# Kernel tuning notes

Hardware: AMD Instinct MI355X
Metric: run time of the kernel (lower is better)

The kernel has to match this reference:

```python
import jax, jax.numpy as jnp
import numpy as np

NUM_STEPS = 50   # global num_steps in source
SCALE = 1000     # global scale in source (fc1 out / fc2 in)
SUBTHRESH = 0.5  # HeavisideBoxcar surrogate half-width
THRESH = 1.0     # firing threshold

@jax.custom_vjp
def heaviside_boxcar(x):
    # spike = H(x); surrogate grad = boxcar of half-width SUBTHRESH
    return (x >= 0.0).astype(x.dtype)

def _hb_fwd(x):
    return heaviside_boxcar(x), x

def _hb_bwd(x, g):
    return (g * (jnp.abs(x) < SUBTHRESH).astype(g.dtype),)

heaviside_boxcar.defvjp(_hb_fwd, _hb_bwd)


def setup_inputs() -> dict:
    key = jax.random.key(0)
    k1, k2, k3 = jax.random.split(key, 3)
    B = 1024
    x = jax.random.uniform(k1, (B, 784), dtype=jnp.float32)  # pixel intensities in [0,1]
    W1 = jax.random.normal(k2, (SCALE, 784), jnp.float32) / np.sqrt(784).astype(np.float32)
    W2 = jax.random.normal(k3, (100, SCALE), jnp.float32) / np.sqrt(SCALE).astype(np.float32)
    tau_0 = jnp.array([2.0], jnp.float32)       # sigmoid(2) ~ 0.88 decay
    tau_vector = jnp.array([2.0], jnp.float32)
    acc_tau = jnp.array([2.0], jnp.float32)
    return {"x": x, "W1": W1, "W2": W2, "tau_0": tau_0,
            "tau_vector": tau_vector, "acc_tau": acc_tau}


def reference(x, W1, W2, tau_0, tau_vector, acc_tau):
    B = x.shape[0]
    # snn.spikegen.rate: per-step Bernoulli(p=x) spikes, shape [T, B, 784]
    u = jax.random.uniform(jax.random.key(42), (NUM_STEPS, B, 784), dtype=x.dtype)
    x_spk = (u < x[None]).astype(x.dtype)

    decay_0 = jax.nn.sigmoid(tau_0[0])
    decay_v = jax.nn.sigmoid(tau_vector[0])
    acc_decay = jax.nn.sigmoid(acc_tau[0])

    h1_mem = jnp.full((B, SCALE), 0.5, x.dtype)
    h1_spk = jnp.zeros((B, SCALE), x.dtype)
    h2_mem = jnp.full((B, 100), 0.5, x.dtype)
    h2_spk = jnp.zeros((B, 100), x.dtype)
    acc = jnp.zeros((B, 10), x.dtype)

    def step(carry, xt):
        h1m, h1s, h2m, h2s, acc = carry
        # pPLIF: mem = mem*decay*(1-spk) + I ; spike = H(mem - thresh)
        h1m = h1m * decay_0 * (1.0 - h1s) + xt @ W1.T
        h1s = heaviside_boxcar(h1m - THRESH)
        h2m = h2m * decay_v * (1.0 - h2s) + h1s @ W2.T
        h2s = heaviside_boxcar(h2m - THRESH)
        boost = jnp.mean(h2s.reshape(B, 10, 10), axis=2)  # AvgPool1d(10,10)
        acc = acc * acc_decay + boost                      # pPLI accumulator
        return (h1m, h1s, h2m, h2s, acc), None

    carry, _ = jax.lax.scan(step, (h1_mem, h1_spk, h2_mem, h2_spk, acc),
                            x_spk[:NUM_STEPS - 1])
    # torch loop runs under no_grad with detach(): block grads through it
    h1m, h1s, h2m, h2s, acc = jax.tree_util.tree_map(jax.lax.stop_gradient, carry)

    # final, differentiable step
    h1m = h1m * decay_0 * (1.0 - h1s) + x_spk[NUM_STEPS - 1] @ W1.T
    h1s = heaviside_boxcar(h1m - THRESH)
    h2m = h2m * decay_v * (1.0 - h2s) + h1s @ W2.T
    h2s = heaviside_boxcar(h2m - THRESH)
    boost = jnp.mean(h2s.reshape(B, 10, 10), axis=2)
    acc = acc * acc_decay + boost
    return acc
```

## Files before the change

### kernel.cpp

```cpp
#include <hip/hip_runtime.h>
#include <hip/hip_bf16.h>
#include <math.h>


#define NSTEPS 50
#define KC1 25
#define NSL 5

typedef __attribute__((ext_vector_type(4)))  int i32x4;
typedef __attribute__((ext_vector_type(16))) int i32x16;

#define OFF_B1     0ull
#define OFF_B2     5111808ull
#define OFF_H1MST  5898240ull
#define OFF_H1SST  14286848ull
#define OFF_H2MST  15335424ull
#define OFF_H2SST  16384000ull
#define OFF_ACCST  16515072ull
#define OFF_AF     16596992ull
#define FIXED_END  59195392ull
#define PERSTEP    8388608ull

#define PREP_BLOCKS 19200

__device__ __forceinline__ unsigned int rotl32(unsigned int v, int d) {
#if __has_builtin(__builtin_amdgcn_alignbit)
  return __builtin_amdgcn_alignbit(v, v, (unsigned int)(32 - d));
#else
  return (v << d) | (v >> (32 - d));
#endif
}

__device__ __forceinline__ unsigned int tf_bits(unsigned int i) {
  const unsigned int ks0 = 0u;
  const unsigned int ks1 = 42u;
  const unsigned int ks2 = 0x1BD11BDAu ^ 0u ^ 42u;
  unsigned int x0 = 0u + ks0;
  unsigned int x1 = i + ks1;
#define TF_RND(r) { x0 += x1; x1 = rotl32(x1, r); x1 ^= x0; }
  TF_RND(13) TF_RND(15) TF_RND(26) TF_RND(6)
  x0 += ks1; x1 += ks2 + 1u;
  TF_RND(17) TF_RND(29) TF_RND(16) TF_RND(24)
  x0 += ks2; x1 += ks0 + 2u;
  TF_RND(13) TF_RND(15) TF_RND(26) TF_RND(6)
  x0 += ks0; x1 += ks1 + 3u;
  TF_RND(17) TF_RND(29) TF_RND(16) TF_RND(24)
  x0 += ks1; x1 += ks2 + 4u;
  TF_RND(13) TF_RND(15) TF_RND(26) TF_RND(6)
  x0 += ks2; x1 += ks0 + 5u;
#undef TF_RND
  return x0 ^ x1;
}

__device__ __forceinline__ void spike_block(
    const float* __restrict__ x, i32x4* __restrict__ A, int t0, int gblk,
    int tid) {
  int g = gblk * 4 + (tid >> 6);
  int lane = tid & 63;
  int kc = g % 25;
  int r = g / 25;
  int mt = r & 31;
  int t = t0 + (r >> 5);
  int b = mt * 32 + (lane & 31);
  int j0 = kc * 32 + ((lane >> 5) << 4);
  unsigned int wds[4] = {0u, 0u, 0u, 0u};
  if (j0 < 784) {
    unsigned int base = (unsigned int)(t * 1024 + b) * 784u + (unsigned int)j0;
    const float* xp = x + b * 784 + j0;
#pragma unroll
    for (int q = 0; q < 4; ++q) {
      float4 xv = *(const float4*)(xp + 4 * q);
      unsigned int K0 = (unsigned int)(int)ceilf(xv.x * 8388608.0f);
      unsigned int K1 = (unsigned int)(int)ceilf(xv.y * 8388608.0f);
      unsigned int K2 = (unsigned int)(int)ceilf(xv.z * 8388608.0f);
      unsigned int K3 = (unsigned int)(int)ceilf(xv.w * 8388608.0f);
      unsigned int w4 = 0u;
      if ((tf_bits(base + 4 * q + 0) >> 9) < K0) w4 |= 1u;
      if ((tf_bits(base + 4 * q + 1) >> 9) < K1) w4 |= 1u << 8;
      if ((tf_bits(base + 4 * q + 2) >> 9) < K2) w4 |= 1u << 16;
      if ((tf_bits(base + 4 * q + 3) >> 9) < K3) w4 |= 1u << 24;
      wds[q] = w4;
    }
  }
  i32x4 v;
  v.x = (int)wds[0]; v.y = (int)wds[1]; v.z = (int)wds[2]; v.w = (int)wds[3];
  A[(size_t)(((t * 32 + mt) * 26) + kc) * 64 + lane] = v;
}

__global__ __launch_bounds__(256) void setup_kernel(
    const float* __restrict__ W1, const float* __restrict__ W2,
    signed char* __restrict__ B1, signed char* __restrict__ B2,
    const float* __restrict__ x, i32x4* __restrict__ A) {
  if (blockIdx.x >= PREP_BLOCKS) {
    spike_block(x, A, 0, blockIdx.x - PREP_BLOCKS, threadIdx.x);
    return;
  }
  int idx = blockIdx.x * 256 + threadIdx.x;
  const int NB1 = NSL * 32 * 26 * 1024;
  const int NB2 = NSL * 4 * 32 * 1024;
  float w;
  int s;
  signed char* dst;
  if (idx < NB1) {
    int jj = idx & 15;
    int lane = (idx >> 4) & 63;
    int kc = (idx >> 10) % 26;
    int rest = (idx >> 10) / 26;
    int nt = rest & 31;
    s = rest >> 5;
    int k = kc * 32 + ((lane >> 5) << 4) + jj;
    int o = nt * 32 + (lane & 31);
    w = (o < 1000 && k < 784) ? W1[o * 784 + k] : 0.0f;
    dst = B1 + idx;
  } else {
    int m = idx - NB1;
    if (m >= NB2) return;
    int jj = m & 15;
    int lane = (m >> 4) & 63;
    int kc = (m >> 10) & 31;
    int rest = (m >> 10) >> 5;
    int nt = rest & 3;
    s = rest >> 2;
    int k = kc * 32 + ((lane >> 5) << 4) + jj;
    int o = nt * 32 + (lane & 31);
    w = (o < 100 && k < 1000) ? W2[o * 1000 + k] : 0.0f;
    dst = B2 + m;
  }
  long long V = llrint((double)w * 281474976710656.0);
  signed char d = 0;
  for (int q = 0; q <= s + 1; ++q) {
    d = (signed char)(V & 0xFF);
    V = (V - (long long)d) >> 8;
  }
  *dst = d;
}

__global__ __launch_bounds__(256, 2) void gemm1_kernel(
    const signed char* __restrict__ Bf, const signed char* __restrict__ Afc,
    int* __restrict__ T1L, short* __restrict__ T1H) {
  __shared__ i32x4 bls[2][NSL][64];
  int tid = threadIdx.x, lane = tid & 63, wv = tid >> 6;
  int id = blockIdx.x;
  int low5 = id & 31;
  int nt = ((low5 & 7) << 2) | ((low5 >> 3) & 3);
  int mg = id >> 5;
  int tl = mg >> 2;
  int q  = mg & 3;
  int mtA = q * 8 + wv * 2;
  const i32x4* ApA = (const i32x4*)Afc + (size_t)((tl * 32 + mtA) * 26) * 64 + lane;
  const i32x4* ApB = ApA + 26 * 64;
  const i32x4* Bp = (const i32x4*)Bf + lane;
#define B1_IDX(s, kc) ((size_t)(((s) * 32 + nt) * 26 + (kc)) * 64)
  const bool st4 = (wv == 0);

  i32x16 CA[NSL], CB[NSL];
#pragma unroll
  for (int s = 0; s < NSL; ++s)
#pragma unroll
    for (int i = 0; i < 16; ++i) { CA[s][i] = 0; CB[s][i] = 0; }

  i32x4 sa = Bp[B1_IDX(wv, 0)];
  i32x4 sb; if (st4) sb = Bp[B1_IDX(4, 0)];
  i32x4 aA0 = ApA[0], aB0 = ApB[0];
  i32x4 aA1 = ApA[64], aB1 = ApB[64];
  i32x4 aA2, aB2;
  bls[0][wv][lane] = sa;
  if (st4) bls[0][4][lane] = sb;
  sa = Bp[B1_IDX(wv, 1)];
  if (st4) sb = Bp[B1_IDX(4, 1)];
  __syncthreads();

  for (int kc = 0; kc < KC1; ++kc) {
    const int cur = kc & 1, nxt = cur ^ 1;
    if (kc + 1 < KC1) {
      bls[nxt][wv][lane] = sa;
      if (st4) bls[nxt][4][lane] = sb;
    }
    if (kc + 2 < KC1) {
      sa = Bp[B1_IDX(wv, kc + 2)];
      if (st4) sb = Bp[B1_IDX(4, kc + 2)];
      aA2 = ApA[(size_t)(kc + 2) * 64];
      aB2 = ApB[(size_t)(kc + 2) * 64];
    }
#pragma unroll
    for (int s = 0; s < NSL; ++s) {
      i32x4 b = bls[cur][s][lane];
      CA[s] = __builtin_amdgcn_mfma_i32_32x32x32_i8(aA0, b, CA[s], 0, 0, 0);
      CB[s] = __builtin_amdgcn_mfma_i32_32x32x32_i8(aB0, b, CB[s], 0, 0, 0);
    }
    __syncthreads();
    aA0 = aA1; aA1 = aA2;
    aB0 = aB1; aB1 = aB2;
  }

  int o = nt * 32 + (lane & 31);
  int rb = 4 * (lane >> 5);
#pragma unroll
  for (int r = 0; r < 16; ++r) {
    int row = (r & 3) + 8 * (r >> 2) + rb;
    long long TA = (long long)CA[4][r];
    TA = (TA << 8) + (long long)CA[3][r];
    TA = (TA << 8) + (long long)CA[2][r];
    TA = (TA << 8) + (long long)CA[1][r];
    TA = (TA << 8) + (long long)CA[0][r];
    long long TB = (long long)CB[4][r];
    TB = (TB << 8) + (long long)CB[3][r];
    TB = (TB << 8) + (long long)CB[2][r];
    TB = (TB << 8) + (long long)CB[1][r];
    TB = (TB << 8) + (long long)CB[0][r];
    int bA = mtA * 32 + row;
    size_t i0 = ((size_t)tl * 1024 + bA) * 1024 + o;
    size_t i1 = ((size_t)tl * 1024 + bA + 32) * 1024 + o;
    T1L[i0] = (int)TA;
    T1H[i0] = (short)(TA >> 32);
    T1L[i1] = (int)TB;
    T1H[i1] = (short)(TB >> 32);
  }
}

__global__ __launch_bounds__(256) void rec1_kernel(
    const int* __restrict__ T1L, const short* __restrict__ T1H,
    signed char* __restrict__ h1sc,
    double* __restrict__ h1m_st, signed char* __restrict__ h1s_st,
    const float* __restrict__ tau0, int t0, int C,
    const float* __restrict__ x, i32x4* __restrict__ A, int t1) {
  if (blockIdx.x >= 512) {
    spike_block(x, A, t1, blockIdx.x - 512, threadIdx.x);
    return;
  }
  int tid = threadIdx.x;
  int lane = tid & 63, sub = tid >> 6;
  int b = blockIdx.x * 2 + (sub >> 1);
  int obase = (sub & 1) * 512 + lane;
  double alpha = 1.0 / (1.0 + exp(-(double)tau0[0]));
  double m[8], s[8];
  if (t0 == 0) {
#pragma unroll
    for (int j = 0; j < 8; ++j) { m[j] = 0.5; s[j] = 0.0; }
  } else {
#pragma unroll
    for (int j = 0; j < 8; ++j) {
      m[j] = h1m_st[(size_t)b * 1024 + obase + 64 * j];
      s[j] = (double)h1s_st[(size_t)b * 1024 + obase + 64 * j];
    }
  }
  for (int tl = 0; tl < C; ++tl) {
    const int*   Lp = T1L + ((size_t)tl * 1024 + b) * 1024 + obase;
    const short* Hp = T1H + ((size_t)tl * 1024 + b) * 1024 + obase;
    signed char* Sp = h1sc + ((size_t)tl * 1024 + b) * 1024 + obase;
#pragma unroll
    for (int j = 0; j < 8; ++j) {
      long long T = ((long long)Hp[64 * j] << 32) +
                    (long long)(unsigned int)Lp[64 * j];
      double I = (double)T * 0x1p-40;
      m[j] = (s[j] != 0.0 ? 0.0 : m[j] * alpha) + I;
      bool sp = (m[j] - 1.0) >= 0.0;
      s[j] = sp ? 1.0 : 0.0;
      Sp[64 * j] = sp ? 1 : 0;
    }
  }
#pragma unroll
  for (int j = 0; j < 8; ++j) {
    h1m_st[(size_t)b * 1024 + obase + 64 * j] = m[j];
    h1s_st[(size_t)b * 1024 + obase + 64 * j] = (signed char)(s[j] != 0.0 ? 1 : 0);
  }
}

__global__ __launch_bounds__(256, 3) void gemm2_kernel(
    const signed char* __restrict__ Bf, const signed char* __restrict__ h1sc,
    double* __restrict__ T2, int ngemm,
    const float* __restrict__ x, i32x4* __restrict__ A, int t1, int gofs) {
  if ((int)blockIdx.x >= ngemm) {
    spike_block(x, A, t1, gofs + (int)blockIdx.x - ngemm, threadIdx.x);
    return;
  }
  __shared__ i32x4 bls[2][NSL][64];
  int tid = threadIdx.x, lane = tid & 63, wv = tid >> 6;
  int nt = blockIdx.x & 3;
  int mg = blockIdx.x >> 2;
  int tl = mg >> 3;
  int mt = ((mg & 7) << 2) + wv;
  const signed char* Arow =
      h1sc + ((size_t)tl * 1024 + mt * 32 + (lane & 31)) * 1024 + ((lane >> 5) << 4);
  const i32x4* Bp = (const i32x4*)Bf + lane;
  const bool st4 = (wv == 0);
#define B2_IDX(s, kc) ((size_t)(((s) * 4 + nt) * 32 + (kc)) * 64)

  i32x16 C[NSL];
#pragma unroll
  for (int s = 0; s < NSL; ++s)
#pragma unroll
    for (int i = 0; i < 16; ++i) C[s][i] = 0;

  i32x4 sa = Bp[B2_IDX(wv, 0)];
  i32x4 sb; if (st4) sb = Bp[B2_IDX(4, 0)];
  i32x4 a0 = *(const i32x4*)(Arow);
  i32x4 a1 = *(const i32x4*)(Arow + 32);
  i32x4 a2;
  bls[0][wv][lane] = sa;
  if (st4) bls[0][4][lane] = sb;
  sa = Bp[B2_IDX(wv, 1)];
  if (st4) sb = Bp[B2_IDX(4, 1)];
  __syncthreads();

  for (int kc = 0; kc < 32; ++kc) {
    const int cur = kc & 1, nxt = cur ^ 1;
    if (kc + 1 < 32) {
      bls[nxt][wv][lane] = sa;
      if (st4) bls[nxt][4][lane] = sb;
    }
    if (kc + 2 < 32) {
      sa = Bp[B2_IDX(wv, kc + 2)];
      if (st4) sb = Bp[B2_IDX(4, kc + 2)];
      a2 = *(const i32x4*)(Arow + (size_t)(kc + 2) * 32);
    }
    i32x4 b0 = bls[cur][0][lane], b1 = bls[cur][1][lane], b2 = bls[cur][2][lane];
    i32x4 b3 = bls[cur][3][lane], b4 = bls[cur][4][lane];
    C[0] = __builtin_amdgcn_mfma_i32_32x32x32_i8(a0, b0, C[0], 0, 0, 0);
    C[1] = __builtin_amdgcn_mfma_i32_32x32x32_i8(a0, b1, C[1], 0, 0, 0);
    C[2] = __builtin_amdgcn_mfma_i32_32x32x32_i8(a0, b2, C[2], 0, 0, 0);
    C[3] = __builtin_amdgcn_mfma_i32_32x32x32_i8(a0, b3, C[3], 0, 0, 0);
    C[4] = __builtin_amdgcn_mfma_i32_32x32x32_i8(a0, b4, C[4], 0, 0, 0);
    a0 = a1; a1 = a2;
    __syncthreads();
  }

  int o = nt * 32 + (lane & 31);
  int rb = 4 * (lane >> 5);
#pragma unroll
  for (int r = 0; r < 16; ++r) {
    int row = (r & 3) + 8 * (r >> 2) + rb;
    int b = mt * 32 + row;
    long long T = (long long)C[4][r];
    T = (T << 8) + (long long)C[3][r];
    T = (T << 8) + (long long)C[2][r];
    T = (T << 8) + (long long)C[1][r];
    T = (T << 8) + (long long)C[0][r];
    T2[((size_t)tl * 1024 + b) * 128 + o] = (double)T * 0x1p-40;
  }
}

__global__ __launch_bounds__(256) void rec2_kernel(
    const double* __restrict__ T2, double* __restrict__ h2m_st,
    signed char* __restrict__ h2s_st, double* __restrict__ acc_st,
    const float* __restrict__ tauv, const float* __restrict__ acct,
    int t0, int C, float* __restrict__ out) {
  __shared__ signed char sp[256];
  int tid = threadIdx.x;
  int b = blockIdx.x * 2 + (tid >> 7);
  int o = tid & 127;
  double alpha = 1.0 / (1.0 + exp(-(double)tauv[0]));
  double adec  = 1.0 / (1.0 + exp(-(double)acct[0]));
  double m, s, accv = 0.0;
  bool isPool = (o < 10);
  if (t0 == 0) {
    m = 0.5; s = 0.0;
  } else {
    m = h2m_st[(size_t)b * 128 + o];
    s = (double)h2s_st[(size_t)b * 128 + o];
    if (isPool) accv = acc_st[b * 10 + o];
  }
  for (int tl = 0; tl < C; ++tl) {
    double I = T2[((size_t)tl * 1024 + b) * 128 + o];
    m = (s != 0.0 ? 0.0 : m * alpha) + I;
    bool spk = (m - 1.0) >= 0.0;
    s = spk ? 1.0 : 0.0;
    sp[tid] = spk ? 1 : 0;
    __syncthreads();
    if (isPool) {
      int base = tid & 128;
      int isum = 0;
#pragma unroll
      for (int k = 0; k < 10; ++k) isum += sp[base + o * 10 + k];
      accv = accv * adec + (double)isum / 10.0;
      if (t0 + tl == NSTEPS - 1) out[b * 10 + o] = (float)accv;
    }
    __syncthreads();
  }
  h2m_st[(size_t)b * 128 + o] = m;
  h2s_st[(size_t)b * 128 + o] = (signed char)(s != 0.0 ? 1 : 0);
  if (isPool) acc_st[b * 10 + o] = accv;
}

extern "C" void kernel_launch(void* const* d_in, const int* in_sizes, int n_in,
                              void* d_out, int out_size, void* d_ws, size_t ws_size,
                              hipStream_t stream) {
  const float* x    = (const float*)d_in[0];
  const float* W1   = (const float*)d_in[1];
  const float* W2   = (const float*)d_in[2];
  const float* tau0 = (const float*)d_in[3];
  const float* tauv = (const float*)d_in[4];
  const float* acct = (const float*)d_in[5];
  float* out = (float*)d_out;
  char*  ws  = (char*)d_ws;

  signed char* B1     = (signed char*)(ws + OFF_B1);
  signed char* B2     = (signed char*)(ws + OFF_B2);
  double*      h1m_st = (double*)(ws + OFF_H1MST);
  signed char* h1s_st = (signed char*)(ws + OFF_H1SST);
  double*      h2m_st = (double*)(ws + OFF_H2MST);
  signed char* h2s_st = (signed char*)(ws + OFF_H2SST);
  double*      acc_st = (double*)(ws + OFF_ACCST);
  signed char* Af     = (signed char*)(ws + OFF_AF);
  i32x4*       Afv    = (i32x4*)Af;

  long long avail = (long long)ws_size - (long long)FIXED_END;
  int C = (int)(avail / (long long)PERSTEP);
  if (C < 1) C = 1;
  if (C > 13) C = 13;
  size_t off_t1l  = FIXED_END;
  size_t off_t1h  = off_t1l + (size_t)C * 4194304ull;
  size_t off_h1sc = off_t1h + (size_t)C * 2097152ull;
  size_t off_t2   = off_h1sc + (size_t)C * 1048576ull;
  int*         T1L  = (int*)(ws + off_t1l);
  short*       T1H  = (short*)(ws + off_t1h);
  signed char* h1sc = (signed char*)(ws + off_h1sc);
  double*      T2   = (double*)(ws + off_t2);

  int C0 = (C < NSTEPS) ? C : NSTEPS;
  setup_kernel<<<PREP_BLOCKS + C0 * 200, 256, 0, stream>>>(
      W1, W2, B1, B2, x, Afv);

  for (int t0 = 0; t0 < NSTEPS; t0 += C) {
    int Cc = (NSTEPS - t0 < C) ? (NSTEPS - t0) : C;
    int t1 = t0 + Cc;
    int Cn = (t1 < NSTEPS) ? ((NSTEPS - t1 < C) ? (NSTEPS - t1) : C) : 0;
    int spkTot = Cn * 200;
    int spkA = spkTot / 2;
    int spkB = spkTot - spkA;
    int ngemm2 = 4 * Cc * 8;

    gemm1_kernel<<<32 * Cc * 4, 256, 0, stream>>>(
        B1, Af + (size_t)t0 * 851968ull, T1L, T1H);
    rec1_kernel<<<512 + spkA, 256, 0, stream>>>(
        T1L, T1H, h1sc, h1m_st, h1s_st, tau0, t0, Cc, x, Afv, t1);
    gemm2_kernel<<<ngemm2 + spkB, 256, 0, stream>>>(
        B2, h1sc, T2, ngemm2, x, Afv, t1, spkA);
    rec2_kernel<<<512, 256, 0, stream>>>(
        T2, h2m_st, h2s_st, acc_st, tauv, acct, t0, Cc, out);
  }
}
```

Baseline: 486.4 us.

## Fuse layer-1 GEMM with recurrence in persistent LDS-resident weight kernel

Replaces the chunked gemm1/rec1 kernel pair with one persistent kernel. Each block keeps its W1 column-tile slices in dynamic shared memory, loops over all 50 timesteps, and applies the membrane/spike recurrence in registers, overlapped with the next step's MFMAs through double-buffered accumulators. This removes the 48-bit T1L/T1H intermediate round-trip to global memory and most kernel launches, and gemm2/rec2 now run once over all steps. In exchange only 256 blocks run the layer-1 chain serially per step. The workspace grows to a fixed large size, and all spike inputs are generated up front in setup.

Measured after the change: 1.298 ms. 2.67x slower.

```diff
diff --git a/kernel.cpp b/kernel.cpp
--- a/kernel.cpp
+++ b/kernel.cpp
@@ -11,17 +11,16 @@
 typedef __attribute__((ext_vector_type(16))) int i32x16;
 
 #define OFF_B1     0ull
-#define OFF_B2     5111808ull
-#define OFF_H1MST  5898240ull
-#define OFF_H1SST  14286848ull
-#define OFF_H2MST  15335424ull
-#define OFF_H2SST  16384000ull
-#define OFF_ACCST  16515072ull
-#define OFF_AF     16596992ull
-#define FIXED_END  59195392ull
-#define PERSTEP    8388608ull
-
-#define PREP_BLOCKS 19200
+#define OFF_B2     4259840ull
+#define OFF_AF     4915200ull
+#define OFF_H1SC   47513600ull
+#define OFF_T2     99942400ull
+#define OFF_H2M    152371200ull
+#define OFF_H2S    153419776ull
+#define OFF_ACC    153550848ull
+#define WS_END     153632768ull
+
+#define PREP_BLOCKS 3840
 
 __device__ __forceinline__ unsigned int rotl32(unsigned int v, int d) {
 #if __has_builtin(__builtin_amdgcn_alignbit)
@@ -96,184 +95,133 @@
     return;
   }
   int idx = blockIdx.x * 256 + threadIdx.x;
-  const int NB1 = NSL * 32 * 26 * 1024;
-  const int NB2 = NSL * 4 * 32 * 1024;
+  const int NB1 = 32 * 26 * 64 * 16;
   float w;
-  int s;
   signed char* dst;
+  size_t stride;
   if (idx < NB1) {
     int jj = idx & 15;
     int lane = (idx >> 4) & 63;
     int kc = (idx >> 10) % 26;
-    int rest = (idx >> 10) / 26;
-    int nt = rest & 31;
-    s = rest >> 5;
+    int nt = (idx >> 10) / 26;
     int k = kc * 32 + ((lane >> 5) << 4) + jj;
     int o = nt * 32 + (lane & 31);
     w = (o < 1000 && k < 784) ? W1[o * 784 + k] : 0.0f;
-    dst = B1 + idx;
+    dst = B1 + (size_t)(nt * 26 + kc) * 5120 + (lane << 4) + jj;
+    stride = 1024;
   } else {
-    int m = idx - NB1;
-    if (m >= NB2) return;
-    int jj = m & 15;
-    int lane = (m >> 4) & 63;
-    int kc = (m >> 10) & 31;
-    int rest = (m >> 10) >> 5;
-    int nt = rest & 3;
-    s = rest >> 2;
+    int m2 = idx - NB1;
+    int jj = m2 & 15;
+    int lane = (m2 >> 4) & 63;
+    int kc = (m2 >> 10) & 31;
+    int nt = (m2 >> 10) >> 5;
     int k = kc * 32 + ((lane >> 5) << 4) + jj;
     int o = nt * 32 + (lane & 31);
     w = (o < 100 && k < 1000) ? W2[o * 1000 + k] : 0.0f;
-    dst = B2 + m;
+    dst = B2 + (size_t)(nt * 32 + kc) * 1024 + (lane << 4) + jj;
+    stride = 4 * 32 * 1024;
   }
   long long V = llrint((double)w * 281474976710656.0);
-  signed char d = 0;
-  for (int q = 0; q <= s + 1; ++q) {
+  signed char d = (signed char)(V & 0xFF);
+  V = (V - (long long)d) >> 8;
+#pragma unroll
+  for (int s = 0; s < 5; ++s) {
     d = (signed char)(V & 0xFF);
     V = (V - (long long)d) >> 8;
-  }
-  *dst = d;
-}
-
-__global__ __launch_bounds__(256, 2) void gemm1_kernel(
-    const signed char* __restrict__ Bf, const signed char* __restrict__ Afc,
-    int* __restrict__ T1L, short* __restrict__ T1H) {
-  __shared__ i32x4 bls[2][NSL][64];
-  int tid = threadIdx.x, lane = tid & 63, wv = tid >> 6;
-  int id = blockIdx.x;
-  int low5 = id & 31;
-  int nt = ((low5 & 7) << 2) | ((low5 >> 3) & 3);
-  int mg = id >> 5;
-  int tl = mg >> 2;
-  int q  = mg & 3;
-  int mtA = q * 8 + wv * 2;
-  const i32x4* ApA = (const i32x4*)Afc + (size_t)((tl * 32 + mtA) * 26) * 64 + lane;
-  const i32x4* ApB = ApA + 26 * 64;
-  const i32x4* Bp = (const i32x4*)Bf + lane;
-#define B1_IDX(s, kc) ((size_t)(((s) * 32 + nt) * 26 + (kc)) * 64)
-  const bool st4 = (wv == 0);
-
-  i32x16 CA[NSL], CB[NSL];
-#pragma unroll
-  for (int s = 0; s < NSL; ++s)
+    dst[(size_t)s * stride] = d;
+  }
+}
+
+#define F1_EPI(CP, r) do {                                                    \
+    long long T = (long long)CP[4][r];                                        \
+    T = (T << 8) + (long long)CP[3][r];                                       \
+    T = (T << 8) + (long long)CP[2][r];                                       \
+    T = (T << 8) + (long long)CP[1][r];                                       \
+    T = (T << 8) + (long long)CP[0][r];                                       \
+    double I = (double)T * 0x1p-40;                                           \
+    double mm = (((spk >> (r)) & 1u) ? 0.0 : m[r] * alpha) + I;               \
+    m[r] = mm;                                                                \
+    unsigned int sp = (mm >= 1.0) ? 1u : 0u;                                  \
+    spk = (spk & ~(1u << (r))) | (sp << (r));                                 \
+    hp[(size_t)(((r) & 3) + 8 * ((r) >> 2) + rb) * 1024] = (signed char)sp;   \
+    CP[0][r] = 0; CP[1][r] = 0; CP[2][r] = 0; CP[3][r] = 0; CP[4][r] = 0;     \
+  } while (0)
+
+#define F1_PHASE(CC, CP, DOEPI) do {                                          \
+    _Pragma("unroll")                                                         \
+    for (int kc = 0; kc < 25; ++kc) {                                         \
+      i32x4 b0 = blsv[(kc * 4 + 0) * 64 + lane];                              \
+      i32x4 b1 = blsv[(kc * 4 + 1) * 64 + lane];                              \
+      i32x4 b2 = blsv[(kc * 4 + 2) * 64 + lane];                              \
+      i32x4 b3 = blsv[(kc * 4 + 3) * 64 + lane];                              \
+      i32x4 av = a0, gv = g0;                                                 \
+      a0 = a1; g0 = g1;                                                       \
+      a1 = (kc + 2 < 25) ? Ap[(kc + 2) * 64]                                  \
+                         : Ap[53248 + (kc + 2 - 25) * 64];                    \
+      g1 = (kc + 2 < 25) ? Bg[((kc + 2) * 5 + 4) * 64]                        \
+                         : Bg[((kc + 2 - 25) * 5 + 4) * 64];                  \
+      CC[0] = __builtin_amdgcn_mfma_i32_32x32x32_i8(av, b0, CC[0], 0, 0, 0);  \
+      CC[1] = __builtin_amdgcn_mfma_i32_32x32x32_i8(av, b1, CC[1], 0, 0, 0);  \
+      CC[2] = __builtin_amdgcn_mfma_i32_32x32x32_i8(av, b2, CC[2], 0, 0, 0);  \
+      CC[3] = __builtin_amdgcn_mfma_i32_32x32x32_i8(av, b3, CC[3], 0, 0, 0);  \
+      CC[4] = __builtin_amdgcn_mfma_i32_32x32x32_i8(av, gv, CC[4], 0, 0, 0);  \
+      if ((DOEPI) && kc < 16) F1_EPI(CP, kc);                                 \
+    }                                                                         \
+    Ap += 53248;                                                              \
+    if (DOEPI) hp += 1048576;                                                 \
+  } while (0)
+
+__global__ __launch_bounds__(256, 1) void fused1_kernel(
+    const signed char* __restrict__ B1, const i32x4* __restrict__ Afc,
+    signed char* __restrict__ h1sc, const float* __restrict__ tau0) {
+  extern __shared__ i32x4 blsv[];
+  const int tid = threadIdx.x, lane = tid & 63, wv = tid >> 6;
+  const int id = (int)blockIdx.x;
+  const int mtg = id & 7, nt = id >> 3;
+  const int mt = mtg * 4 + wv;
+  const i32x4* B1v = (const i32x4*)B1;
+
+  for (int r = tid; r < 6400; r += 256) {
+    int fi = r >> 6, l = r & 63;
+    int kc = fi >> 2, s = fi & 3;
+    blsv[r] = B1v[(size_t)nt * 8320 + (kc * 5 + s) * 64 + l];
+  }
+
+  const double alpha = 1.0 / (1.0 + exp(-(double)tau0[0]));
+  double m[16];
+  unsigned int spk = 0;
+#pragma unroll
+  for (int r = 0; r < 16; ++r) m[r] = 0.5;
+  i32x16 CA[5], CB[5];
+#pragma unroll
+  for (int s = 0; s < 5; ++s)
 #pragma unroll
     for (int i = 0; i < 16; ++i) { CA[s][i] = 0; CB[s][i] = 0; }
 
-  i32x4 sa = Bp[B1_IDX(wv, 0)];
-  i32x4 sb; if (st4) sb = Bp[B1_IDX(4, 0)];
-  i32x4 aA0 = ApA[0], aB0 = ApB[0];
-  i32x4 aA1 = ApA[64], aB1 = ApB[64];
-  i32x4 aA2, aB2;
-  bls[0][wv][lane] = sa;
-  if (st4) bls[0][4][lane] = sb;
-  sa = Bp[B1_IDX(wv, 1)];
-  if (st4) sb = Bp[B1_IDX(4, 1)];
+  const i32x4* Ap = Afc + (size_t)mt * 26 * 64 + lane;
+  const i32x4* Bg = B1v + (size_t)nt * 8320 + lane;
+  const int rb = 4 * (lane >> 5);
+  signed char* hp = h1sc + (size_t)(mt * 32) * 1024 + nt * 32 + (lane & 31);
+
   __syncthreads();
 
-  for (int kc = 0; kc < KC1; ++kc) {
-    const int cur = kc & 1, nxt = cur ^ 1;
-    if (kc + 1 < KC1) {
-      bls[nxt][wv][lane] = sa;
-      if (st4) bls[nxt][4][lane] = sb;
-    }
-    if (kc + 2 < KC1) {
-      sa = Bp[B1_IDX(wv, kc + 2)];
-      if (st4) sb = Bp[B1_IDX(4, kc + 2)];
-      aA2 = ApA[(size_t)(kc + 2) * 64];
-      aB2 = ApB[(size_t)(kc + 2) * 64];
-    }
-#pragma unroll
-    for (int s = 0; s < NSL; ++s) {
-      i32x4 b = bls[cur][s][lane];
-      CA[s] = __builtin_amdgcn_mfma_i32_32x32x32_i8(aA0, b, CA[s], 0, 0, 0);
-      CB[s] = __builtin_amdgcn_mfma_i32_32x32x32_i8(aB0, b, CB[s], 0, 0, 0);
-    }
-    __syncthreads();
-    aA0 = aA1; aA1 = aA2;
-    aB0 = aB1; aB1 = aB2;
-  }
-
-  int o = nt * 32 + (lane & 31);
-  int rb = 4 * (lane >> 5);
-#pragma unroll
-  for (int r = 0; r < 16; ++r) {
-    int row = (r & 3) + 8 * (r >> 2) + rb;
-    long long TA = (long long)CA[4][r];
-    TA = (TA << 8) + (long long)CA[3][r];
-    TA = (TA << 8) + (long long)CA[2][r];
-    TA = (TA << 8) + (long long)CA[1][r];
-    TA = (TA << 8) + (long long)CA[0][r];
-    long long TB = (long long)CB[4][r];
-    TB = (TB << 8) + (long long)CB[3][r];
-    TB = (TB << 8) + (long long)CB[2][r];
-    TB = (TB << 8) + (long long)CB[1][r];
-    TB = (TB << 8) + (long long)CB[0][r];
-    int bA = mtA * 32 + row;
-    size_t i0 = ((size_t)tl * 1024 + bA) * 1024 + o;
-    size_t i1 = ((size_t)tl * 1024 + bA + 32) * 1024 + o;
-    T1L[i0] = (int)TA;
-    T1H[i0] = (short)(TA >> 32);
-    T1L[i1] = (int)TB;
-    T1H[i1] = (short)(TB >> 32);
-  }
-}
-
-__global__ __launch_bounds__(256) void rec1_kernel(
-    const int* __restrict__ T1L, const short* __restrict__ T1H,
-    signed char* __restrict__ h1sc,
-    double* __restrict__ h1m_st, signed char* __restrict__ h1s_st,
-    const float* __restrict__ tau0, int t0, int C,
-    const float* __restrict__ x, i32x4* __restrict__ A, int t1) {
-  if (blockIdx.x >= 512) {
-    spike_block(x, A, t1, blockIdx.x - 512, threadIdx.x);
-    return;
-  }
-  int tid = threadIdx.x;
-  int lane = tid & 63, sub = tid >> 6;
-  int b = blockIdx.x * 2 + (sub >> 1);
-  int obase = (sub & 1) * 512 + lane;
-  double alpha = 1.0 / (1.0 + exp(-(double)tau0[0]));
-  double m[8], s[8];
-  if (t0 == 0) {
-#pragma unroll
-    for (int j = 0; j < 8; ++j) { m[j] = 0.5; s[j] = 0.0; }
-  } else {
-#pragma unroll
-    for (int j = 0; j < 8; ++j) {
-      m[j] = h1m_st[(size_t)b * 1024 + obase + 64 * j];
-      s[j] = (double)h1s_st[(size_t)b * 1024 + obase + 64 * j];
-    }
-  }
-  for (int tl = 0; tl < C; ++tl) {
-    const int*   Lp = T1L + ((size_t)tl * 1024 + b) * 1024 + obase;
-    const short* Hp = T1H + ((size_t)tl * 1024 + b) * 1024 + obase;
-    signed char* Sp = h1sc + ((size_t)tl * 1024 + b) * 1024 + obase;
-#pragma unroll
-    for (int j = 0; j < 8; ++j) {
-      long long T = ((long long)Hp[64 * j] << 32) +
-                    (long long)(unsigned int)Lp[64 * j];
-      double I = (double)T * 0x1p-40;
-      m[j] = (s[j] != 0.0 ? 0.0 : m[j] * alpha) + I;
-      bool sp = (m[j] - 1.0) >= 0.0;
-      s[j] = sp ? 1.0 : 0.0;
-      Sp[64 * j] = sp ? 1 : 0;
-    }
-  }
-#pragma unroll
-  for (int j = 0; j < 8; ++j) {
-    h1m_st[(size_t)b * 1024 + obase + 64 * j] = m[j];
-    h1s_st[(size_t)b * 1024 + obase + 64 * j] = (signed char)(s[j] != 0.0 ? 1 : 0);
-  }
+  i32x4 a0 = Ap[0], a1 = Ap[64];
+  i32x4 g0 = Bg[4 * 64], g1 = Bg[9 * 64];
+
+  F1_PHASE(CA, CB, 0);
+#pragma unroll 1
+  for (int tp = 0; tp < 24; ++tp) {
+    F1_PHASE(CB, CA, 1);
+    F1_PHASE(CA, CB, 1);
+  }
+  F1_PHASE(CB, CA, 1);
+#pragma unroll
+  for (int r = 0; r < 16; ++r) F1_EPI(CB, r);
 }
 
 __global__ __launch_bounds__(256, 3) void gemm2_kernel(
     const signed char* __restrict__ Bf, const signed char* __restrict__ h1sc,
-    double* __restrict__ T2, int ngemm,
-    const float* __restrict__ x, i32x4* __restrict__ A, int t1, int gofs) {
-  if ((int)blockIdx.x >= ngemm) {
-    spike_block(x, A, t1, gofs + (int)blockIdx.x - ngemm, threadIdx.x);
-    return;
-  }
+    double* __restrict__ T2) {
   __shared__ i32x4 bls[2][NSL][64];
   int tid = threadIdx.x, lane = tid & 63, wv = tid >> 6;
   int nt = blockIdx.x & 3;
@@ -396,47 +344,29 @@
 
   signed char* B1     = (signed char*)(ws + OFF_B1);
   signed char* B2     = (signed char*)(ws + OFF_B2);
-  double*      h1m_st = (double*)(ws + OFF_H1MST);
-  signed char* h1s_st = (signed char*)(ws + OFF_H1SST);
-  double*      h2m_st = (double*)(ws + OFF_H2MST);
-  signed char* h2s_st = (signed char*)(ws + OFF_H2SST);
-  double*      acc_st = (double*)(ws + OFF_ACCST);
   signed char* Af     = (signed char*)(ws + OFF_AF);
+  signed char* h1sc   = (signed char*)(ws + OFF_H1SC);
+  double*      T2     = (double*)(ws + OFF_T2);
+  double*      h2m_st = (double*)(ws + OFF_H2M);
+  signed char* h2s_st = (signed char*)(ws + OFF_H2S);
+  double*      acc_st = (double*)(ws + OFF_ACC);
   i32x4*       Afv    = (i32x4*)Af;
 
-  long long avail = (long long)ws_size - (long long)FIXED_END;
-  int C = (int)(avail / (long long)PERSTEP);
-  if (C < 1) C = 1;
-  if (C > 13) C = 13;
-  size_t off_t1l  = FIXED_END;
-  size_t off_t1h  = off_t1l + (size_t)C * 4194304ull;
-  size_t off_h1sc = off_t1h + (size_t)C * 2097152ull;
-  size_t off_t2   = off_h1sc + (size_t)C * 1048576ull;
-  int*         T1L  = (int*)(ws + off_t1l);
-  short*       T1H  = (short*)(ws + off_t1h);
-  signed char* h1sc = (signed char*)(ws + off_h1sc);
-  double*      T2   = (double*)(ws + off_t2);
-
-  int C0 = (C < NSTEPS) ? C : NSTEPS;
-  setup_kernel<<<PREP_BLOCKS + C0 * 200, 256, 0, stream>>>(
+  static bool attr_done = false;
+  if (!attr_done) {
+    (void)hipFuncSetAttribute((const void*)fused1_kernel,
+                              hipFuncAttributeMaxDynamicSharedMemorySize,
+                              102400);
+    attr_done = true;
+  }
+
+  setup_kernel<<<PREP_BLOCKS + NSTEPS * 200, 256, 0, stream>>>(
       W1, W2, B1, B2, x, Afv);
 
-  for (int t0 = 0; t0 < NSTEPS; t0 += C) {
-    int Cc = (NSTEPS - t0 < C) ? (NSTEPS - t0) : C;
-    int t1 = t0 + Cc;
-    int Cn = (t1 < NSTEPS) ? ((NSTEPS - t1 < C) ? (NSTEPS - t1) : C) : 0;
-    int spkTot = Cn * 200;
-    int spkA = spkTot / 2;
-    int spkB = spkTot - spkA;
-    int ngemm2 = 4 * Cc * 8;
-
-    gemm1_kernel<<<32 * Cc * 4, 256, 0, stream>>>(
-        B1, Af + (size_t)t0 * 851968ull, T1L, T1H);
-    rec1_kernel<<<512 + spkA, 256, 0, stream>>>(
-        T1L, T1H, h1sc, h1m_st, h1s_st, tau0, t0, Cc, x, Afv, t1);
-    gemm2_kernel<<<ngemm2 + spkB, 256, 0, stream>>>(
-        B2, h1sc, T2, ngemm2, x, Afv, t1, spkA);
-    rec2_kernel<<<512, 256, 0, stream>>>(
-        T2, h2m_st, h2s_st, acc_st, tauv, acct, t0, Cc, out);
-  }
-}
+  fused1_kernel<<<256, 256, 102400, stream>>>(B1, Afv, h1sc, tau0);
+
+  gemm2_kernel<<<4 * NSTEPS * 8, 256, 0, stream>>>(B2, h1sc, T2);
+
+  rec2_kernel<<<512, 256, 0, stream>>>(
+      T2, h2m_st, h2s_st, acc_st, tauv, acct, 0, NSTEPS, out);
+}
```
